# Optimization experiments

Hardware: AMD Instinct MI355X
Metric: run time of the kernel (lower is better)

Reference implementation:

```python
import jax, jax.numpy as jnp
import numpy as np

L = 4          # dilation_depth
HID = 32       # hidden_channels
F_IN = 16
F_OUT = 16
K = 2          # conv kernel size


def setup_inputs() -> dict:
    key = jax.random.key(0)
    ks = jax.random.split(key, 20)
    B, T, N, F = 8, 512, 128, F_IN
    s = 0.1
    inp = {
        "X": jax.random.normal(ks[0], (B, T, N, F), jnp.float32),
        "A": jax.random.normal(ks[1], (N, N), jnp.float32) / jnp.sqrt(N).astype(jnp.float32),
        "in_w": jax.random.normal(ks[2], (F, 3 * HID), jnp.float32) * s,
        "in_b": jnp.zeros((3 * HID,), jnp.float32),
        "ct_w": jax.random.normal(ks[3], (L, K, HID, HID), jnp.float32) * s,
        "ct_b": jnp.zeros((L, HID), jnp.float32),
        "cs_w": jax.random.normal(ks[4], (L, K, HID, HID), jnp.float32) * s,
        "cs_b": jnp.zeros((L, HID), jnp.float32),
        "gcn_w": jax.random.normal(ks[5], (L, HID, HID), jnp.float32) * s,
        "gcn_b": jnp.zeros((L, HID), jnp.float32),
        "res_w": jax.random.normal(ks[6], (L, HID, HID), jnp.float32) * s,
        "res_b": jnp.zeros((L, HID), jnp.float32),
        "skip_w": jax.random.normal(ks[7], (L, HID, HID), jnp.float32) * s,
        "skip_b": jnp.zeros((L, HID), jnp.float32),
        "out1_w": jax.random.normal(ks[8], (HID, HID), jnp.float32) * s,
        "out1_b": jnp.zeros((HID,), jnp.float32),
        "out2_w": jax.random.normal(ks[9], (HID, F_OUT), jnp.float32) * s,
        "out2_b": jnp.zeros((F_OUT,), jnp.float32),
    }
    return inp


def _causal_conv(x, w, b, dilation):
    # x: [BN, T, C]; w: [K, C_in, C_out] (WIO); causal pad left by dilation*(K-1)
    pad = dilation * (w.shape[0] - 1)
    y = jax.lax.conv_general_dilated(
        x, w, window_strides=(1,), padding=[(pad, 0)],
        rhs_dilation=(dilation,), dimension_numbers=("NWC", "WIO", "NWC"))
    return y + b


def reference(X, A, in_w, in_b, ct_w, ct_b, cs_w, cs_b, gcn_w, gcn_b,
              res_w, res_b, skip_w, skip_b, out1_w, out1_b, out2_w, out2_b):
    B, T, N, F = X.shape
    Xp = X @ in_w + in_b                      # [B,T,N,3H]
    x_a, x_b, x_res = jnp.split(Xp, 3, axis=-1)
    H = x_a.shape[-1]
    # Faithful to source: raw reshape [B,T,N,H] -> [B*N,T,H] (no transpose), as in the original code.
    x_a_r = x_a.reshape(B * N, T, H)
    x_b_r = x_b.reshape(B * N, T, H)
    skip = jnp.zeros_like(x_res)
    for i in range(L):
        d = 2 ** i
        tcn = (jnp.tanh(_causal_conv(x_a_r, ct_w[i], ct_b[i], d))
               * jax.nn.sigmoid(_causal_conv(x_b_r, cs_w[i], cs_b[i], d)))
        tcn = tcn.reshape(B, N, T, H).transpose(0, 2, 1, 3)   # [B,T,N,H]
        gcn = jnp.einsum('ij,btjf->btif', A, x_res) @ gcn_w[i] + gcn_b[i]
        h = tcn + gcn
        x_res = (h @ res_w[i] + res_b[i]) + x_res
        skip = skip + (h @ skip_w[i] + skip_b[i])
    h = jax.nn.relu(skip)
    h = jax.nn.relu(h @ out1_w + out1_b)
    return h @ out2_w + out2_b
```

## Files before the change

### kernel.cpp

```cpp
#include <hip/hip_runtime.h>
#include <math.h>

#define T_ 512

typedef _Float16 half8 __attribute__((ext_vector_type(8)));
typedef _Float16 half4 __attribute__((ext_vector_type(4)));
typedef float f32x4 __attribute__((ext_vector_type(4)));

__device__ __forceinline__ float ts_act(float a, float b) {
    float e2a = __expf(a + a);
    float eb  = __expf(b);
    float num = (e2a - 1.0f) * eb;
    float den = (e2a + 1.0f) * (eb + 1.0f);
    return num * __builtin_amdgcn_rcpf(den);
}

__device__ __forceinline__ half4 pack4(f32x4 v) {
    half4 h;
    h[0] = (_Float16)v[0]; h[1] = (_Float16)v[1];
    h[2] = (_Float16)v[2]; h[3] = (_Float16)v[3];
    return h;
}

__global__ __launch_bounds__(256) void k_prep(
    const float* __restrict__ A,     const float* __restrict__ in_w,
    const float* __restrict__ in_b,
    const float* __restrict__ ct_w,  const float* __restrict__ ct_b,
    const float* __restrict__ cs_w,  const float* __restrict__ cs_b,
    const float* __restrict__ gcn_w, const float* __restrict__ res_w,
    const float* __restrict__ skip_w,
    const float* __restrict__ out1_w,const float* __restrict__ out2_w,
    _Float16* __restrict__ FR, float* __restrict__ BIAS)
{
    int idx = blockIdx.x * 256 + threadIdx.x;
    if (idx < 16384) {
        int j = idx & 7, L = (idx >> 3) & 63, tile = idx >> 9;
        int it = tile >> 2, kt = tile & 3;
        FR[idx] = (_Float16)A[(it * 16 + (L & 15)) * 128 + kt * 32 + (L >> 4) * 8 + j];
    } else if (idx < 24576) {
        int e = idx - 16384;
        int j = e & 7, L = (e >> 3) & 63, ct = (e >> 9) & 1, mat = e >> 10;
        int k = (L >> 4) * 8 + j, col = ct * 16 + (L & 15);
        int l = mat >> 1, br = mat & 1;
        const float* tw = (br ? cs_w : ct_w) + l * 2048;
        int bro = br * 32;
        float v = 0.f;
        if (k < 16) { for (int c = 0; c < 32; ++c) v += in_w[k*96 + bro + c] * tw[c*32 + col]; }
        else        { for (int c = 0; c < 32; ++c) v += in_w[(k-16)*96 + bro + c] * tw[1024 + c*32 + col]; }
        FR[idx] = (_Float16)v;
    } else if (idx < 39936) {
        int e = idx - 24576;
        int i = e & 3, L = (e >> 2) & 63, ct = (e >> 8) & 1, ks = (e >> 9) & 1, mat = e >> 10;
        int k = ks * 16 + (L >> 4) * 4 + i, col = ct * 16 + (L & 15);
        float v;
        if (mat < 12) {
            int l = mat / 3, r = mat - l * 3;
            const float* W = (r == 0) ? gcn_w : (r == 1) ? res_w : skip_w;
            v = W[l * 1024 + k * 32 + col];
        } else if (mat == 12) v = out1_w[k * 32 + col];
        else if (mat == 13)   v = (ct == 0) ? out2_w[k * 16 + (L & 15)] : 0.f;
        else                  v = (ks == 0) ? in_w[k * 96 + 64 + col] : 0.f;
        FR[idx] = (_Float16)v;
    } else if (idx < 40448) {
        int e = idx - 39936;
        int n = e & 31, br = (e >> 5) & 1, pvi = (e >> 6) & 1, l = e >> 7;
        const float* W  = br ? cs_w : ct_w;
        const float* bb = br ? cs_b : ct_b;
        int ibo = br * 32;
        float v = bb[l * 32 + n];
        for (int c = 0; c < 32; ++c) v += in_b[ibo + c] * W[l*2048 + 1024 + c*32 + n];
        if (pvi)
            for (int c = 0; c < 32; ++c) v += in_b[ibo + c] * W[l*2048 + c*32 + n];
        BIAS[e] = v;
    }
}

__global__ __launch_bounds__(256, 3) void k_fused(
    const float* __restrict__ X,
    const _Float16* __restrict__ FR,
    const float* __restrict__ BIAS,
    const float* __restrict__ in_b,
    const float* __restrict__ gcn_b,
    const float* __restrict__ res_b,
    const float* __restrict__ skip_b,
    const float* __restrict__ b1,
    const float* __restrict__ b2,
    float* __restrict__ out)
{
    __shared__ _Float16 Pld[128 * 40];
    __shared__ _Float16 xsT[2][32 * 136];

    const int bx = blockIdx.x;
    const int btid = ((bx & 7) << 9) | (bx >> 3);
    const int b = btid >> 9, t = btid & (T_ - 1);
    const int tid = threadIdx.x, lane = tid & 63, w = tid >> 6;
    const int lm = lane & 15, kb = lane >> 4;
    const int R = w * 32;

    const half8* AFv  = (const half8*)FR;
    const half8* W32v = (const half8*)(FR + 16384);
    const half4* W16v = (const half4*)(FR + 24576);
    const f32x4 zero4 = {0.f, 0.f, 0.f, 0.f};

    const int row = lane >> 1, ch = lane & 1;

    f32x4 xm[2][2], skT[2][2];
    {
        const float4 x0 = *(const float4*)(X + ((size_t)btid * 128 + R + lm) * 16 + kb * 4);
        const float4 x1 = *(const float4*)(X + ((size_t)btid * 128 + R + 16 + lm) * 16 + kb * 4);
        half4 p0, p1;
        p0[0]=(_Float16)x0.x; p0[1]=(_Float16)x0.y; p0[2]=(_Float16)x0.z; p0[3]=(_Float16)x0.w;
        p1[0]=(_Float16)x1.x; p1[1]=(_Float16)x1.y; p1[2]=(_Float16)x1.z; p1[3]=(_Float16)x1.w;
#pragma unroll
        for (int f = 0; f < 2; ++f) {
            half4 wi = W16v[(56 + f) * 64 + lane];
            float bi = in_b[64 + f * 16 + lm];
            f32x4 cb; cb[0] = bi; cb[1] = bi; cb[2] = bi; cb[3] = bi;
            xm[0][f] = __builtin_amdgcn_mfma_f32_16x16x16f16(p0, wi, cb, 0, 0, 0);
            xm[1][f] = __builtin_amdgcn_mfma_f32_16x16x16f16(p1, wi, cb, 0, 0, 0);
        }
#pragma unroll
        for (int f3 = 0; f3 < 2; ++f3) {
            f32x4 s = zero4;
#pragma unroll
            for (int l = 0; l < 4; ++l) {
                const float4 q = *(const float4*)&skip_b[l * 32 + f3 * 16 + kb * 4];
                s[0] += q.x; s[1] += q.y; s[2] += q.z; s[3] += q.w;
            }
            skT[f3][0] = s; skT[f3][1] = s;
        }
    }

    {
        const float4* s4 = (const float4*)(X + ((size_t)(b * 128 + R + row) * T_ + t) * 16 + ch * 8);
        float4 u0 = s4[0], u1 = s4[1];
        half8 hv;
        hv[0]=(_Float16)u0.x; hv[1]=(_Float16)u0.y; hv[2]=(_Float16)u0.z; hv[3]=(_Float16)u0.w;
        hv[4]=(_Float16)u1.x; hv[5]=(_Float16)u1.y; hv[6]=(_Float16)u1.z; hv[7]=(_Float16)u1.w;
        *(half8*)&Pld[(R + row) * 40 + 16 + ch * 8] = hv;
    }

#pragma unroll 1
    for (int l = 0; l < 4; ++l) {
        const int d = 1 << l;
        const bool pv = (t >= d);
        const float* B2 = BIAS + (l * 2 + (pv ? 1 : 0)) * 64;

        {
            half8 hv = {0,0,0,0,0,0,0,0};
            if (pv) {
                const float4* s4 = (const float4*)(X + ((size_t)(b * 128 + R + row) * T_ + (t - d)) * 16 + ch * 8);
                float4 u0 = s4[0], u1 = s4[1];
                hv[0]=(_Float16)u0.x; hv[1]=(_Float16)u0.y; hv[2]=(_Float16)u0.z; hv[3]=(_Float16)u0.w;
                hv[4]=(_Float16)u1.x; hv[5]=(_Float16)u1.y; hv[6]=(_Float16)u1.z; hv[7]=(_Float16)u1.w;
            }
            *(half8*)&Pld[(R + row) * 40 + ch * 8] = hv;
        }

        half8 pf0 = *(const half8*)&Pld[(R + lm) * 40 + kb * 8];
        half8 pf1 = *(const half8*)&Pld[(R + 16 + lm) * 40 + kb * 8];
        f32x4 tcv[2][2];
#pragma unroll
        for (int ct = 0; ct < 2; ++ct) {
            half8 wt = W32v[((l * 2 + 0) * 2 + ct) * 64 + lane];
            half8 ws = W32v[((l * 2 + 1) * 2 + ct) * 64 + lane];
            const f32x4 cT = *(const f32x4*)&B2[ct * 16 + kb * 4];
            const f32x4 cS = *(const f32x4*)&B2[32 + ct * 16 + kb * 4];
            f32x4 dt0 = __builtin_amdgcn_mfma_f32_16x16x32_f16(wt, pf0, cT, 0, 0, 0);
            f32x4 dt1 = __builtin_amdgcn_mfma_f32_16x16x32_f16(wt, pf1, cT, 0, 0, 0);
            f32x4 ds0 = __builtin_amdgcn_mfma_f32_16x16x32_f16(ws, pf0, cS, 0, 0, 0);
            f32x4 ds1 = __builtin_amdgcn_mfma_f32_16x16x32_f16(ws, pf1, cS, 0, 0, 0);
#pragma unroll
            for (int r = 0; r < 4; ++r) {
                tcv[ct][0][r] = ts_act(dt0[r], ds0[r]);
                tcv[ct][1][r] = ts_act(dt1[r], ds1[r]);
            }
        }

        const int buf = l & 1;
#pragma unroll
        for (int mt = 0; mt < 2; ++mt)
#pragma unroll
            for (int f = 0; f < 2; ++f)
                *(half4*)&xsT[buf][(f * 16 + lm) * 136 + R + mt * 16 + kb * 4] = pack4(xm[mt][f]);
        __syncthreads();

        f32x4 AxT[2][2];
        half8 Afr[2][4];
#pragma unroll
        for (int mt = 0; mt < 2; ++mt)
#pragma unroll
            for (int kt = 0; kt < 4; ++kt)
                Afr[mt][kt] = AFv[((w * 2 + mt) * 4 + kt) * 64 + lane];
#pragma unroll
        for (int f = 0; f < 2; ++f) {
            half8 xa[4];
#pragma unroll
            for (int kt = 0; kt < 4; ++kt)
                xa[kt] = *(const half8*)&xsT[buf][(f * 16 + lm) * 136 + kt * 32 + kb * 8];
#pragma unroll
            for (int mt = 0; mt < 2; ++mt) {
                f32x4 acc = zero4;
#pragma unroll
                for (int kt = 0; kt < 4; ++kt)
                    acc = __builtin_amdgcn_mfma_f32_16x16x32_f16(xa[kt], Afr[mt][kt], acc, 0, 0, 0);
                AxT[f][mt] = acc;
            }
        }

        half4 axh[2][2];
#pragma unroll
        for (int f = 0; f < 2; ++f)
#pragma unroll
            for (int mt = 0; mt < 2; ++mt) axh[f][mt] = pack4(AxT[f][mt]);
        half4 hh[2][2];
#pragma unroll
        for (int g = 0; g < 2; ++g) {
            half4 gw0 = W16v[((l * 3 + 0) * 4 + 0 + g) * 64 + lane];
            half4 gw1 = W16v[((l * 3 + 0) * 4 + 2 + g) * 64 + lane];
            const f32x4 gq = *(const f32x4*)&gcn_b[l * 32 + g * 16 + kb * 4];
#pragma unroll
            for (int mt = 0; mt < 2; ++mt) {
                f32x4 acc = __builtin_amdgcn_mfma_f32_16x16x16f16(gw0, axh[0][mt], gq, 0, 0, 0);
                acc = __builtin_amdgcn_mfma_f32_16x16x16f16(gw1, axh[1][mt], acc, 0, 0, 0);
#pragma unroll
                for (int r = 0; r < 4; ++r) acc[r] += tcv[g][mt][r];
                hh[g][mt] = pack4(acc);
            }
        }

#pragma unroll
        for (int mt = 0; mt < 2; ++mt)
#pragma unroll
            for (int f3 = 0; f3 < 2; ++f3) {
                half4 rw0 = W16v[((l * 3 + 1) * 4 + 0 + f3) * 64 + lane];
                half4 rw1 = W16v[((l * 3 + 1) * 4 + 2 + f3) * 64 + lane];
                f32x4 acc = __builtin_amdgcn_mfma_f32_16x16x16f16(hh[0][mt], rw0, xm[mt][f3], 0, 0, 0);
                xm[mt][f3] = __builtin_amdgcn_mfma_f32_16x16x16f16(hh[1][mt], rw1, acc, 0, 0, 0);
                float rb = res_b[l * 32 + f3 * 16 + lm];
#pragma unroll
                for (int r = 0; r < 4; ++r) xm[mt][f3][r] += rb;

                half4 sw0 = W16v[((l * 3 + 2) * 4 + 0 + f3) * 64 + lane];
                half4 sw1 = W16v[((l * 3 + 2) * 4 + 2 + f3) * 64 + lane];
                f32x4 acs = __builtin_amdgcn_mfma_f32_16x16x16f16(sw0, hh[0][mt], skT[f3][mt], 0, 0, 0);
                skT[f3][mt] = __builtin_amdgcn_mfma_f32_16x16x16f16(sw1, hh[1][mt], acs, 0, 0, 0);
            }
    }

    half4 rs[2][2];
#pragma unroll
    for (int g = 0; g < 2; ++g)
#pragma unroll
        for (int mt = 0; mt < 2; ++mt) {
            f32x4 v;
#pragma unroll
            for (int r = 0; r < 4; ++r) v[r] = fmaxf(skT[g][mt][r], 0.f);
            rs[g][mt] = pack4(v);
        }
    half4 h1h[2][2];
#pragma unroll
    for (int g4 = 0; g4 < 2; ++g4) {
        half4 w10 = W16v[(48 + 0 + g4) * 64 + lane];
        half4 w11 = W16v[(48 + 2 + g4) * 64 + lane];
        const f32x4 bq = *(const f32x4*)&b1[g4 * 16 + kb * 4];
#pragma unroll
        for (int mt = 0; mt < 2; ++mt) {
            f32x4 acc = __builtin_amdgcn_mfma_f32_16x16x16f16(w10, rs[0][mt], bq, 0, 0, 0);
            acc = __builtin_amdgcn_mfma_f32_16x16x16f16(w11, rs[1][mt], acc, 0, 0, 0);
            f32x4 v;
#pragma unroll
            for (int r = 0; r < 4; ++r) v[r] = fmaxf(acc[r], 0.f);
            h1h[g4][mt] = pack4(v);
        }
    }
    {
        half4 w20 = W16v[(52 + 0) * 64 + lane];
        half4 w21 = W16v[(52 + 2) * 64 + lane];
        const f32x4 b2q = *(const f32x4*)&b2[kb * 4];
#pragma unroll
        for (int mt = 0; mt < 2; ++mt) {
            f32x4 acc = __builtin_amdgcn_mfma_f32_16x16x16f16(w20, h1h[0][mt], b2q, 0, 0, 0);
            acc = __builtin_amdgcn_mfma_f32_16x16x16f16(w21, h1h[1][mt], acc, 0, 0, 0);
            float4 o = make_float4(acc[0], acc[1], acc[2], acc[3]);
            *(float4*)&out[((size_t)btid * 128 + R + mt * 16 + lm) * 16 + kb * 4] = o;
        }
    }
}

extern "C" void kernel_launch(void* const* d_in, const int* in_sizes, int n_in,
                              void* d_out, int out_size, void* d_ws, size_t ws_size,
                              hipStream_t stream)
{
    const float* X      = (const float*)d_in[0];
    const float* A      = (const float*)d_in[1];
    const float* in_w   = (const float*)d_in[2];
    const float* in_b   = (const float*)d_in[3];
    const float* ct_w   = (const float*)d_in[4];
    const float* ct_b   = (const float*)d_in[5];
    const float* cs_w   = (const float*)d_in[6];
    const float* cs_b   = (const float*)d_in[7];
    const float* gcn_w  = (const float*)d_in[8];
    const float* gcn_b  = (const float*)d_in[9];
    const float* res_w  = (const float*)d_in[10];
    const float* res_b  = (const float*)d_in[11];
    const float* skip_w = (const float*)d_in[12];
    const float* skip_b = (const float*)d_in[13];
    const float* out1_w = (const float*)d_in[14];
    const float* out1_b = (const float*)d_in[15];
    const float* out2_w = (const float*)d_in[16];
    const float* out2_b = (const float*)d_in[17];

    _Float16* FR   = (_Float16*)d_ws;
    float*    BIAS = (float*)((char*)d_ws + 79872);

    k_prep<<<158, 256, 0, stream>>>(A, in_w, in_b, ct_w, ct_b, cs_w, cs_b,
                                    gcn_w, res_w, skip_w, out1_w, out2_w,
                                    FR, BIAS);

    k_fused<<<8 * T_, 256, 0, stream>>>(X, FR, BIAS, in_b,
                                        gcn_b, res_b, skip_b,
                                        out1_b, out2_b, (float*)d_out);
}
```

Baseline: 198.5 us.

## Preload all dilated time-step inputs upfront and interleave conv MFMAs with graph matmul

Loads the current and all four dilated past time-step rows of X into an enlarged shared buffer once, before the layer loop, instead of issuing a global load inside each layer. The layer loop is reordered so the xsT stores, A-fragment and bias loads happen before the barrier. The causal-conv MFMAs are issued before the graph matmul, and the tanh-sigmoid activation is deferred until after it. This aims to hide global load latency and overlap transcendental math with MFMA work, at the cost of more shared memory and more live registers, which may reduce occupancy.

```diff
diff --git a/kernel.cpp b/kernel.cpp
--- a/kernel.cpp
+++ b/kernel.cpp
@@ -87,7 +87,7 @@
     const float* __restrict__ b2,
     float* __restrict__ out)
 {
-    __shared__ _Float16 Pld[128 * 40];
+    __shared__ _Float16 Pld[128 * 88];
     __shared__ _Float16 xsT[2][32 * 136];
 
     const int bx = blockIdx.x;
@@ -96,13 +96,40 @@
     const int tid = threadIdx.x, lane = tid & 63, w = tid >> 6;
     const int lm = lane & 15, kb = lane >> 4;
     const int R = w * 32;
+    const int row = lane >> 1, ch = lane & 1;
 
     const half8* AFv  = (const half8*)FR;
     const half8* W32v = (const half8*)(FR + 16384);
     const half4* W16v = (const half4*)(FR + 24576);
     const f32x4 zero4 = {0.f, 0.f, 0.f, 0.f};
 
-    const int row = lane >> 1, ch = lane & 1;
+    {
+        const size_t nrow = (size_t)(b * 128 + R + row) * T_;
+        const float4* xc = (const float4*)(X + (nrow + t) * 16 + ch * 8);
+        float4 c0 = xc[0], c1 = xc[1];
+        float4 p0[4], p1[4];
+#pragma unroll
+        for (int l = 0; l < 4; ++l) {
+            const int d = 1 << l;
+            if (t >= d) {
+                const float4* xp = (const float4*)(X + (nrow + (t - d)) * 16 + ch * 8);
+                p0[l] = xp[0]; p1[l] = xp[1];
+            } else {
+                p0[l] = make_float4(0.f, 0.f, 0.f, 0.f);
+                p1[l] = make_float4(0.f, 0.f, 0.f, 0.f);
+            }
+        }
+        half8 hv;
+        hv[0]=(_Float16)c0.x; hv[1]=(_Float16)c0.y; hv[2]=(_Float16)c0.z; hv[3]=(_Float16)c0.w;
+        hv[4]=(_Float16)c1.x; hv[5]=(_Float16)c1.y; hv[6]=(_Float16)c1.z; hv[7]=(_Float16)c1.w;
+        *(half8*)&Pld[(R + row) * 88 + 64 + ch * 8] = hv;
+#pragma unroll
+        for (int l = 0; l < 4; ++l) {
+            hv[0]=(_Float16)p0[l].x; hv[1]=(_Float16)p0[l].y; hv[2]=(_Float16)p0[l].z; hv[3]=(_Float16)p0[l].w;
+            hv[4]=(_Float16)p1[l].x; hv[5]=(_Float16)p1[l].y; hv[6]=(_Float16)p1[l].z; hv[7]=(_Float16)p1[l].w;
+            *(half8*)&Pld[(R + row) * 88 + l * 16 + ch * 8] = hv;
+        }
+    }
 
     f32x4 xm[2][2], skT[2][2];
     {
@@ -131,67 +158,51 @@
         }
     }
 
-    {
-        const float4* s4 = (const float4*)(X + ((size_t)(b * 128 + R + row) * T_ + t) * 16 + ch * 8);
-        float4 u0 = s4[0], u1 = s4[1];
-        half8 hv;
-        hv[0]=(_Float16)u0.x; hv[1]=(_Float16)u0.y; hv[2]=(_Float16)u0.z; hv[3]=(_Float16)u0.w;
-        hv[4]=(_Float16)u1.x; hv[5]=(_Float16)u1.y; hv[6]=(_Float16)u1.z; hv[7]=(_Float16)u1.w;
-        *(half8*)&Pld[(R + row) * 40 + 16 + ch * 8] = hv;
-    }
+    const int fragoff = (kb < 2) ? kb * 8 : 64 + (kb - 2) * 8;
+    const int lstep   = (kb < 2) ? 16 : 0;
 
 #pragma unroll 1
     for (int l = 0; l < 4; ++l) {
-        const int d = 1 << l;
-        const bool pv = (t >= d);
+        const bool pv = (t >= (1 << l));
         const float* B2 = BIAS + (l * 2 + (pv ? 1 : 0)) * 64;
-
-        {
-            half8 hv = {0,0,0,0,0,0,0,0};
-            if (pv) {
-                const float4* s4 = (const float4*)(X + ((size_t)(b * 128 + R + row) * T_ + (t - d)) * 16 + ch * 8);
-                float4 u0 = s4[0], u1 = s4[1];
-                hv[0]=(_Float16)u0.x; hv[1]=(_Float16)u0.y; hv[2]=(_Float16)u0.z; hv[3]=(_Float16)u0.w;
-                hv[4]=(_Float16)u1.x; hv[5]=(_Float16)u1.y; hv[6]=(_Float16)u1.z; hv[7]=(_Float16)u1.w;
-            }
-            *(half8*)&Pld[(R + row) * 40 + ch * 8] = hv;
-        }
-
-        half8 pf0 = *(const half8*)&Pld[(R + lm) * 40 + kb * 8];
-        half8 pf1 = *(const half8*)&Pld[(R + 16 + lm) * 40 + kb * 8];
-        f32x4 tcv[2][2];
+        const int buf = l & 1;
+
+#pragma unroll
+        for (int mt = 0; mt < 2; ++mt)
+#pragma unroll
+            for (int f = 0; f < 2; ++f)
+                *(half4*)&xsT[buf][(f * 16 + lm) * 136 + R + mt * 16 + kb * 4] = pack4(xm[mt][f]);
+
+        half8 Afr[2][4];
+#pragma unroll
+        for (int mt = 0; mt < 2; ++mt)
+#pragma unroll
+            for (int kt = 0; kt < 4; ++kt)
+                Afr[mt][kt] = AFv[((w * 2 + mt) * 4 + kt) * 64 + lane];
+        const f32x4 cT0 = *(const f32x4*)&B2[0 * 16 + kb * 4];
+        const f32x4 cT1 = *(const f32x4*)&B2[1 * 16 + kb * 4];
+        const f32x4 cS0 = *(const f32x4*)&B2[32 + 0 * 16 + kb * 4];
+        const f32x4 cS1 = *(const f32x4*)&B2[32 + 1 * 16 + kb * 4];
+
+        __syncthreads();
+
+        const int poff = fragoff + l * lstep;
+        half8 pf0 = *(const half8*)&Pld[(R + lm) * 88 + poff];
+        half8 pf1 = *(const half8*)&Pld[(R + 16 + lm) * 88 + poff];
+        f32x4 dt[2][2], ds[2][2];
 #pragma unroll
         for (int ct = 0; ct < 2; ++ct) {
             half8 wt = W32v[((l * 2 + 0) * 2 + ct) * 64 + lane];
             half8 ws = W32v[((l * 2 + 1) * 2 + ct) * 64 + lane];
-            const f32x4 cT = *(const f32x4*)&B2[ct * 16 + kb * 4];
-            const f32x4 cS = *(const f32x4*)&B2[32 + ct * 16 + kb * 4];
-            f32x4 dt0 = __builtin_amdgcn_mfma_f32_16x16x32_f16(wt, pf0, cT, 0, 0, 0);
-            f32x4 dt1 = __builtin_amdgcn_mfma_f32_16x16x32_f16(wt, pf1, cT, 0, 0, 0);
-            f32x4 ds0 = __builtin_amdgcn_mfma_f32_16x16x32_f16(ws, pf0, cS, 0, 0, 0);
-            f32x4 ds1 = __builtin_amdgcn_mfma_f32_16x16x32_f16(ws, pf1, cS, 0, 0, 0);
-#pragma unroll
-            for (int r = 0; r < 4; ++r) {
-                tcv[ct][0][r] = ts_act(dt0[r], ds0[r]);
-                tcv[ct][1][r] = ts_act(dt1[r], ds1[r]);
-            }
-        }
-
-        const int buf = l & 1;
-#pragma unroll
-        for (int mt = 0; mt < 2; ++mt)
-#pragma unroll
-            for (int f = 0; f < 2; ++f)
-                *(half4*)&xsT[buf][(f * 16 + lm) * 136 + R + mt * 16 + kb * 4] = pack4(xm[mt][f]);
-        __syncthreads();
+            const f32x4 cT = ct ? cT1 : cT0;
+            const f32x4 cS = ct ? cS1 : cS0;
+            dt[ct][0] = __builtin_amdgcn_mfma_f32_16x16x32_f16(wt, pf0, cT, 0, 0, 0);
+            dt[ct][1] = __builtin_amdgcn_mfma_f32_16x16x32_f16(wt, pf1, cT, 0, 0, 0);
+            ds[ct][0] = __builtin_amdgcn_mfma_f32_16x16x32_f16(ws, pf0, cS, 0, 0, 0);
+            ds[ct][1] = __builtin_amdgcn_mfma_f32_16x16x32_f16(ws, pf1, cS, 0, 0, 0);
+        }
 
         f32x4 AxT[2][2];
-        half8 Afr[2][4];
-#pragma unroll
-        for (int mt = 0; mt < 2; ++mt)
-#pragma unroll
-            for (int kt = 0; kt < 4; ++kt)
-                Afr[mt][kt] = AFv[((w * 2 + mt) * 4 + kt) * 64 + lane];
 #pragma unroll
         for (int f = 0; f < 2; ++f) {
             half8 xa[4];
@@ -207,6 +218,15 @@
                 AxT[f][mt] = acc;
             }
         }
+
+        f32x4 tcv[2][2];
+#pragma unroll
+        for (int ct = 0; ct < 2; ++ct)
+#pragma unroll
+            for (int mt = 0; mt < 2; ++mt)
+#pragma unroll
+                for (int r = 0; r < 4; ++r)
+                    tcv[ct][mt][r] = ts_act(dt[ct][mt][r], ds[ct][mt][r]);
 
         half4 axh[2][2];
 #pragma unroll
```

New measurement: 195.6 us. No clear change (-1.5%).
